# Performance work log

Measured on AMD Instinct MI355X. Metric: run time of the kernel, lower is better.

Reference implementation:

```python
import jax, jax.numpy as jnp
import numpy as np

P = 10          # num_patches
EPS = 1e-20
ALPHAS = dict(stretch=1.0, E=1.0, G=1.0, skew=1.0, total_area=1.0, total_area_mult=1.0)
ALPHA_MC = 1.0
ALPHA_DISTORT = 1.0


def setup_inputs() -> dict:
    key = jax.random.key(0)
    k1, k2, k3, k4 = jax.random.split(key, 4)
    B, N, M = 8, 8192, 2500
    pc_gt = jax.random.normal(k1, (B, N, 3), dtype=jnp.float32)
    pc_pred = jax.random.normal(k2, (B, M, 3), dtype=jnp.float32)
    # first fundamental form (E, F, G); ensure E*G - F^2 > 0 so sqrt is smooth
    u = jax.random.uniform(k3, (B, M, 3), dtype=jnp.float32)
    fff = u * 0.5 + jnp.array([1.0, 0.0, 1.0], dtype=jnp.float32)
    A_gt = jax.random.uniform(k4, (B,), dtype=jnp.float32)
    return {"pc_gt": pc_gt, "pc_pred": pc_pred, "fff": fff, "A_gt": A_gt}


def _forward(pc_gt, pc_pred, fff, A_gt):
    B, M, _ = pc_pred.shape
    spp = M // P

    # ---- Chamfer distance via dense (B, M, N) distance matrix + argmin ----
    diff = pc_pred[:, :, None, :] - pc_gt[:, None, :, :]          # (B, M, N, 3)
    distm = jnp.sqrt(jnp.sum(diff * diff, axis=3))                # (B, M, N)
    inds_p2gt = jnp.argmin(distm, axis=2)                         # (B, M)
    inds_gt2p = jnp.argmin(distm, axis=1)                         # (B, N)
    pc_gt_reg = jnp.take_along_axis(pc_gt, inds_p2gt[..., None], axis=1)   # (B, M, 3)
    pc_p_reg = jnp.take_along_axis(pc_pred, inds_gt2p[..., None], axis=1)  # (B, N, 3)
    d_p2gt = jnp.sum((pc_pred - pc_gt_reg) ** 2, axis=2)
    d_gt2p = jnp.sum((pc_gt - pc_p_reg) ** 2, axis=2)
    L_chd = d_p2gt.mean() + d_gt2p.mean()

    # ---- FFF-based losses ----
    EFG = jnp.transpose(fff.reshape(B, P, spp, 3), (3, 0, 1, 2))  # (3, B, P, spp)
    E, F, G = EFG[0], EFG[1], EFG[2]

    # metric consistency between consecutive frame pairs
    Eh = E.reshape(B // 2, 2, P, spp)
    Fh = F.reshape(B // 2, 2, P, spp)
    Gh = G.reshape(B // 2, 2, P, spp)
    L_mc = ((Eh[:, 0] - Eh[:, 1]) ** 2
            + 2.0 * (Fh[:, 0] - Fh[:, 1]) ** 2
            + (Gh[:, 0] - Gh[:, 1]) ** 2).mean()

    # scaled isometry (collapse) losses
    A2 = jnp.maximum(E * G - F * F, 0.0)                          # (B, P, spp)
    A = jnp.sqrt(A2)
    inv = 1.0 / (A2 + EPS)
    L_stretch = (((E - G) ** 2) * inv).mean() * ALPHAS['stretch']
    L_E = (((E - E.mean()) ** 2) * inv).mean() * ALPHAS['E']
    L_G = (((G - G.mean()) ** 2) * inv).mean() * ALPHAS['G']
    L_F = ((F * F) * inv).mean() * ALPHAS['skew']

    # overlap / total-area loss
    A_tot = A.mean(axis=2).sum(axis=1)                            # (B,)
    L_olap = (jnp.maximum(0.0, A_tot - A_gt * ALPHAS['total_area_mult']) ** 2).mean() * ALPHAS['total_area']

    loss_sciso = L_F + L_E + L_G + L_stretch + L_olap
    loss_tot = L_chd + ALPHA_MC * L_mc + ALPHA_DISTORT * loss_sciso
    return loss_tot


def reference(pc_gt, pc_pred, fff, A_gt):
    return _forward(pc_gt, pc_pred, fff, A_gt)
```

## Files before the change

kernel.cpp:

```cpp
#include <hip/hip_runtime.h>

#define B_   8
#define N_   8192
#define M_   2500
#define SPP_ 250
#define EPS_ 1e-20f
#define BIGF 1e30f

#define NB_P2GT 640
#define NB_GT2P 512
#define NB_FFF1 79
#define NB_K1   (NB_P2GT + NB_GT2P + NB_FFF1)

#define NB_RG2P 256
#define NB_RP2  79
#define NB_FFF2 79
#define NB_K2   (NB_RG2P + NB_RP2 + NB_FFF2)

#define WS_P2GT 0
#define WS_GT2P 160000
#define WS_F1P  291072
#define WS_RED  292336
#define RO_G2P  0
#define RO_P2   256
#define RO_EC   335
#define RO_GC   414
#define WS_CNT  292829

typedef __attribute__((ext_vector_type(8)))  short short8_t;
typedef __attribute__((ext_vector_type(4)))  float float4_t;

__device__ __forceinline__ unsigned pack_bf2(float lo, float hi) {
    unsigned a = __float_as_uint(lo);
    unsigned b = __float_as_uint(hi);
    a = (a + 0x7FFFu + ((a >> 16) & 1u)) >> 16;
    b = (b + 0x7FFFu + ((b >> 16) & 1u)) & 0xFFFF0000u;
    return a | b;
}
__device__ __forceinline__ short bf16s(float x) {
    unsigned a = __float_as_uint(x);
    return (short)((a + 0x7FFFu + ((a >> 16) & 1u)) >> 16);
}

__device__ __forceinline__ float wave_sum64(float v) {
    #pragma unroll
    for (int o = 32; o > 0; o >>= 1) v += __shfl_down(v, o, 64);
    return v;
}
__device__ __forceinline__ float block_sum256(float v, float* red4) {
    v = wave_sum64(v);
    int wid  = threadIdx.x >> 6;
    int lane = threadIdx.x & 63;
    if (lane == 0) red4[wid] = v;
    __syncthreads();
    float r = 0.f;
    if (threadIdx.x == 0) r = red4[0] + red4[1] + red4[2] + red4[3];
    __syncthreads();
    return r;
}

__device__ __forceinline__ void min4(float4_t& c, const float4_t d) {
    c.x = fminf(c.x, d.x); c.y = fminf(c.y, d.y);
    c.z = fminf(c.z, d.z); c.w = fminf(c.w, d.w);
}
__device__ __forceinline__ void quad_min4(float4_t& c) {
    #pragma unroll
    for (int m = 1; m < 16; m <<= 1) {
        c.x = fminf(c.x, __shfl_xor(c.x, m, 64));
        c.y = fminf(c.y, __shfl_xor(c.y, m, 64));
        c.z = fminf(c.z, __shfl_xor(c.z, m, 64));
        c.w = fminf(c.w, __shfl_xor(c.w, m, 64));
    }
}

__global__ void __launch_bounds__(256) k1_main(
        const float* __restrict__ gt, const float* __restrict__ pred,
        const float* __restrict__ fff, float* __restrict__ ws) {
    __shared__ uint4 spts[1280];
    __shared__ __align__(16) float saux[256];
    const int bid = blockIdx.x;
    const int tid = threadIdx.x;
    const int lane = tid & 63;
    const int w    = tid >> 6;
    const int quad = lane >> 4;
    const int l15  = lane & 15;

    if (bid == 0 && tid == 0) ((unsigned*)(ws + WS_CNT))[0] = 0u;

    if (bid < NB_P2GT + NB_GT2P) {
        const bool is_p2gt = bid < NB_P2GT;
        int b, mblk, z, ntiles, nstage, blim, alim;
        const float* apts; const float* bpts; float* dst;
        if (is_p2gt) {
            z = bid / 80; int rem = bid % 80;
            b = rem / 10; mblk = rem % 10;
            apts = pred + (size_t)b * M_ * 3;
            bpts = gt + ((size_t)b * N_ + (size_t)z * 1024) * 3;
            ntiles = 64; nstage = 1024; blim = 1024; alim = M_;
            dst = ws + WS_P2GT + (size_t)z * 20000 + b * M_;
        } else {
            int r = bid - NB_P2GT;
            z = r >> 8; int rem = r & 255;
            b = rem >> 5; mblk = rem & 31;
            apts = gt + (size_t)b * N_ * 3;
            bpts = pred + ((size_t)b * M_ + (size_t)z * 1280) * 3;
            ntiles = 80; nstage = 1280; blim = M_ - z * 1280; alim = N_;
            dst = ws + WS_GT2P + (size_t)z * 65536 + b * N_;
        }
        const int abase = mblk * 256 + w * 64;

        for (int i = tid; i < nstage; i += 256) {
            float x = 0.f, y = 0.f, zc = 0.f, n2 = BIGF;
            if (i < blim) {
                x = bpts[i * 3 + 0]; y = bpts[i * 3 + 1]; zc = bpts[i * 3 + 2];
                n2 = x * x + y * y + zc * zc;
            }
            uint4 q;
            q.x = pack_bf2(-2.f * x, -2.f * y);
            q.y = pack_bf2(-2.f * zc, n2);
            q.z = q.x; q.w = q.y;
            spts[i] = q;
        }

        short8_t af[4];
        #pragma unroll
        for (int t = 0; t < 4; ++t) af[t] = (short8_t){0,0,0,0,0,0,0,0};
        if (lane < 16) {
            #pragma unroll
            for (int t = 0; t < 4; ++t) {
                int m = abase + t * 16 + l15;
                int c = m < alim ? m : alim - 1;
                float x = apts[c*3+0], y = apts[c*3+1], zc = apts[c*3+2];
                af[t][0] = bf16s(x); af[t][1] = bf16s(y); af[t][2] = bf16s(zc);
                af[t][3] = (short)0x3F80;
                saux[w * 64 + t * 16 + l15] = x*x + y*y + zc*zc;
            }
        }
        __syncthreads();

        const float4_t* bp = (const float4_t*)saux;
        float4_t bias[4];
        #pragma unroll
        for (int t = 0; t < 4; ++t) bias[t] = bp[w * 16 + t * 4 + quad];

        float4_t c[4];
        #pragma unroll
        for (int t = 0; t < 4; ++t) c[t] = (float4_t){BIGF, BIGF, BIGF, BIGF};

        const uint4* bptr = spts + l15;
        #pragma unroll 4
        for (int i = 0; i < ntiles; ++i) {
            short8_t bf = __builtin_bit_cast(short8_t, bptr[i * 16]);
            #pragma unroll
            for (int t = 0; t < 4; ++t) {
                float4_t d = __builtin_amdgcn_mfma_f32_16x16x32_bf16(
                                 af[t], bf, bias[t], 0, 0, 0);
                min4(c[t], d);
            }
        }
        #pragma unroll
        for (int t = 0; t < 4; ++t) quad_min4(c[t]);

        if (l15 == 0) {
            #pragma unroll
            for (int t = 0; t < 4; ++t) {
                int m0 = abase + t * 16 + quad * 4;
                if (m0 < alim)
                    *(float4_t*)(dst + m0) = c[t];
            }
        }
    } else {
        const int kb = bid - NB_P2GT - NB_GT2P;
        const int i  = kb * 256 + tid;
        float* red4 = saux;
        float* sA   = saux + 8;
        if (tid < B_) sA[tid] = 0.f;
        __syncthreads();

        float sE = 0.f, sG = 0.f, sMC = 0.f, sST = 0.f, sF = 0.f;
        if (i < B_ * M_) {
            const int b = i / M_;
            const int m = i - b * M_;
            const float* f = fff + (size_t)i * 3;
            float E = f[0], F = f[1], G = f[2];
            sE = E; sG = G;
            float A2  = fmaxf(E * G - F * F, 0.f);
            float inv = 1.f / (A2 + EPS_);
            sST = (E - G) * (E - G) * inv;
            sF  = F * F * inv;
            atomicAdd(&sA[b], sqrtf(A2));
            if ((b & 1) == 0) {
                const float* f2 = fff + ((size_t)(b + 1) * M_ + m) * 3;
                float dE = E - f2[0], dF = F - f2[1], dG = G - f2[2];
                sMC = dE * dE + 2.f * dF * dF + dG * dG;
            }
        }
        float rE  = block_sum256(sE,  red4);
        float rG  = block_sum256(sG,  red4);
        float rMC = block_sum256(sMC, red4);
        float rST = block_sum256(sST, red4);
        float rF  = block_sum256(sF,  red4);
        float* outp = ws + WS_F1P + (size_t)kb * 16;
        if (tid == 0) {
            outp[0] = rE; outp[1] = rG; outp[2] = rMC; outp[3] = rST; outp[4] = rF;
        }
        __syncthreads();
        if (tid < B_) outp[5 + tid] = sA[tid];
    }
}

__global__ void __launch_bounds__(256) k2_reduce(
        const float* __restrict__ fff, const float* __restrict__ A_gt,
        float* __restrict__ ws, float* __restrict__ out) {
    __shared__ float red4[4];
    __shared__ float bc2[2];
    const int bid = blockIdx.x;
    const int tid = threadIdx.x;
    float* redp = ws + WS_RED;
    const float* f1p = ws + WS_F1P;

    if (bid < NB_RG2P) {
        const int o = bid * 256 + tid;
        const float* src = ws + WS_GT2P + o;
        float m = fminf(src[0], src[65536]);
        float r = block_sum256(fmaxf(m, 0.f), red4);
        if (tid == 0) redp[RO_G2P + bid] = r;
    } else if (bid < NB_RG2P + NB_RP2) {
        const int kb = bid - NB_RG2P;
        const int o = kb * 256 + tid;
        float s = 0.f;
        if (o < 20000) {
            const float* src = ws + WS_P2GT + o;
            float m = src[0];
            #pragma unroll
            for (int zz = 1; zz < 8; ++zz) m = fminf(m, src[zz * 20000]);
            s = fmaxf(m, 0.f);
        }
        float r = block_sum256(s, red4);
        if (tid == 0) redp[RO_P2 + kb] = r;
    } else {
        const int kb = bid - NB_RG2P - NB_RP2;
        float pe = 0.f, pg = 0.f;
        if (tid < 79) { pe = f1p[tid * 16 + 0]; pg = f1p[tid * 16 + 1]; }
        float rE = block_sum256(pe, red4);
        float rG = block_sum256(pg, red4);
        if (tid == 0) { bc2[0] = rE; bc2[1] = rG; }
        __syncthreads();
        const float mE = bc2[0] * (1.f / 20000.f);
        const float mG = bc2[1] * (1.f / 20000.f);

        const int i = kb * 256 + tid;
        float sEC = 0.f, sGC = 0.f;
        if (i < B_ * M_) {
            const float* f = fff + (size_t)i * 3;
            float E = f[0], F = f[1], G = f[2];
            float A2  = fmaxf(E * G - F * F, 0.f);
            float inv = 1.f / (A2 + EPS_);
            sEC = (E - mE) * (E - mE) * inv;
            sGC = (G - mG) * (G - mG) * inv;
        }
        float rEC = block_sum256(sEC, red4);
        float rGC = block_sum256(sGC, red4);
        if (tid == 0) { redp[RO_EC + kb] = rEC; redp[RO_GC + kb] = rGC; }
    }

    __syncthreads();
    if (tid == 0) __threadfence();
    __syncthreads();
    __shared__ unsigned old_s;
    if (tid == 0)
        old_s = __hip_atomic_fetch_add((unsigned*)(ws + WS_CNT), 1u,
                                       __ATOMIC_ACQ_REL, __HIP_MEMORY_SCOPE_AGENT);
    __syncthreads();
    if (old_s == (unsigned)(NB_K2 - 1)) {
        float v;
        v = redp[RO_G2P + tid];
        float sGT2P = block_sum256(v, red4);
        v = (tid < 79) ? redp[RO_P2 + tid] : 0.f;
        float sP2GT = block_sum256(v, red4);
        v = (tid < 79) ? redp[RO_EC + tid] : 0.f;
        float sEC = block_sum256(v, red4);
        v = (tid < 79) ? redp[RO_GC + tid] : 0.f;
        float sGC = block_sum256(v, red4);
        v = (tid < 79) ? f1p[tid * 16 + 2] : 0.f;
        float sMC = block_sum256(v, red4);
        v = (tid < 79) ? f1p[tid * 16 + 3] : 0.f;
        float sST = block_sum256(v, red4);
        v = (tid < 79) ? f1p[tid * 16 + 4] : 0.f;
        float sF = block_sum256(v, red4);
        float sAb[B_];
        #pragma unroll
        for (int b = 0; b < B_; ++b) {
            v = (tid < 79) ? f1p[tid * 16 + 5 + b] : 0.f;
            sAb[b] = block_sum256(v, red4);
        }
        if (tid == 0) {
            float L_chd = sP2GT * (1.f / 20000.f) + sGT2P * (1.f / 65536.f);
            float L_mc  = sMC * (1.f / 10000.f);
            float L_sc  = (sST + sF + sEC + sGC) * (1.f / 20000.f);
            float L_olap = 0.f;
            #pragma unroll
            for (int b = 0; b < B_; ++b) {
                float At = sAb[b] * (1.f / (float)SPP_);
                float r  = fmaxf(0.f, At - A_gt[b]);
                L_olap += r * r;
            }
            L_olap *= (1.f / (float)B_);
            out[0] = L_chd + L_mc + L_sc + L_olap;
        }
    }
}

extern "C" void kernel_launch(void* const* d_in, const int* in_sizes, int n_in,
                              void* d_out, int out_size, void* d_ws, size_t ws_size,
                              hipStream_t stream) {
    const float* pc_gt   = (const float*)d_in[0];
    const float* pc_pred = (const float*)d_in[1];
    const float* fff     = (const float*)d_in[2];
    const float* A_gt    = (const float*)d_in[3];
    float* ws  = (float*)d_ws;
    float* out = (float*)d_out;

    k1_main  <<<NB_K1, 256, 0, stream>>>(pc_gt, pc_pred, fff, ws);
    k2_reduce<<<NB_K2, 256, 0, stream>>>(fff, A_gt, ws, out);
}
```

Baseline: 107.6 us.

## Fuse reduction kernel into main kernel with per-tile counters and algebraic variance expansion

Merges the two kernels into one. Per-row-block atomic counters let the last z-slice block compute the min-across-slices and its partial sum, and a global counter lets the last block finish the loss. The E/G centered losses are expanded algebraically into raw moment sums (E^2*inv, E*inv, inv), so the second pass over fff is gone. Each wave now handles 8 MFMA row tiles instead of 4, which halves block counts. A memset launch is added, and the expanded form risks cancellation error.

Measured after the change: 153.2 us. +42.5%, slower.

```diff
diff --git a/kernel.cpp b/kernel.cpp
--- a/kernel.cpp
+++ b/kernel.cpp
@@ -7,28 +7,34 @@
 #define EPS_ 1e-20f
 #define BIGF 1e30f
 
-#define NB_P2GT 640
-#define NB_GT2P 512
-#define NB_FFF1 79
-#define NB_K1   (NB_P2GT + NB_GT2P + NB_FFF1)
-
-#define NB_RG2P 256
-#define NB_RP2  79
-#define NB_FFF2 79
-#define NB_K2   (NB_RG2P + NB_RP2 + NB_FFF2)
+#define NB_P2GT 320
+#define NB_GT2P 256
+#define NB_FFF  79
+#define NB_ALL  (NB_P2GT + NB_GT2P + NB_FFF)
 
 #define WS_P2GT 0
 #define WS_GT2P 160000
-#define WS_F1P  291072
-#define WS_RED  292336
-#define RO_G2P  0
-#define RO_P2   256
-#define RO_EC   335
-#define RO_GC   414
-#define WS_CNT  292829
-
-typedef __attribute__((ext_vector_type(8)))  short short8_t;
-typedef __attribute__((ext_vector_type(4)))  float float4_t;
+#define WS_ACC  291072
+#define WS_GC   291092
+#define GC_P2   0
+#define GC_G2   40
+#define GC_ALL  168
+#define A_P2   0
+#define A_G2   1
+#define A_E    2
+#define A_G    3
+#define A_MC   4
+#define A_ST   5
+#define A_F2I  6
+#define A_E2I  7
+#define A_EI   8
+#define A_G2I  9
+#define A_GI   10
+#define A_I    11
+#define A_AB   12
+
+typedef __attribute__((ext_vector_type(8))) short short8_t;
+typedef __attribute__((ext_vector_type(4))) float float4_t;
 
 __device__ __forceinline__ unsigned pack_bf2(float lo, float hi) {
     unsigned a = __float_as_uint(lo);
@@ -41,16 +47,14 @@
     unsigned a = __float_as_uint(x);
     return (short)((a + 0x7FFFu + ((a >> 16) & 1u)) >> 16);
 }
-
 __device__ __forceinline__ float wave_sum64(float v) {
     #pragma unroll
     for (int o = 32; o > 0; o >>= 1) v += __shfl_down(v, o, 64);
     return v;
 }
-__device__ __forceinline__ float block_sum256(float v, float* red4) {
+__device__ __forceinline__ float block_sum256(float v, volatile float* red4) {
     v = wave_sum64(v);
-    int wid  = threadIdx.x >> 6;
-    int lane = threadIdx.x & 63;
+    int wid = threadIdx.x >> 6, lane = threadIdx.x & 63;
     if (lane == 0) red4[wid] = v;
     __syncthreads();
     float r = 0.f;
@@ -58,7 +62,6 @@
     __syncthreads();
     return r;
 }
-
 __device__ __forceinline__ void min4(float4_t& c, const float4_t d) {
     c.x = fminf(c.x, d.x); c.y = fminf(c.y, d.y);
     c.z = fminf(c.z, d.z); c.w = fminf(c.w, d.w);
@@ -73,41 +76,46 @@
     }
 }
 
-__global__ void __launch_bounds__(256) k1_main(
+__global__ void __launch_bounds__(256) fused_all(
         const float* __restrict__ gt, const float* __restrict__ pred,
-        const float* __restrict__ fff, float* __restrict__ ws) {
+        const float* __restrict__ fff, const float* __restrict__ A_gt,
+        float* __restrict__ ws, float* __restrict__ out) {
     __shared__ uint4 spts[1280];
-    __shared__ __align__(16) float saux[256];
+    __shared__ __align__(16) float saux[516];
+    __shared__ bool isred;
     const int bid = blockIdx.x;
     const int tid = threadIdx.x;
     const int lane = tid & 63;
     const int w    = tid >> 6;
     const int quad = lane >> 4;
     const int l15  = lane & 15;
-
-    if (bid == 0 && tid == 0) ((unsigned*)(ws + WS_CNT))[0] = 0u;
+    float* acc = ws + WS_ACC;
+    unsigned* gc = (unsigned*)(ws + WS_GC);
 
     if (bid < NB_P2GT + NB_GT2P) {
         const bool is_p2gt = bid < NB_P2GT;
-        int b, mblk, z, ntiles, nstage, blim, alim;
+        int b, mblk, z, ntiles, blim, alim, gidx, nz;
         const float* apts; const float* bpts; float* dst;
         if (is_p2gt) {
-            z = bid / 80; int rem = bid % 80;
-            b = rem / 10; mblk = rem % 10;
+            z = bid / 40; int rem = bid % 40;
+            b = rem / 5;  mblk = rem % 5;
             apts = pred + (size_t)b * M_ * 3;
             bpts = gt + ((size_t)b * N_ + (size_t)z * 1024) * 3;
-            ntiles = 64; nstage = 1024; blim = 1024; alim = M_;
-            dst = ws + WS_P2GT + (size_t)z * 20000 + b * M_;
+            ntiles = 64; blim = 1024; alim = M_;
+            dst  = ws + WS_P2GT + (size_t)z * 20000 + b * M_;
+            gidx = GC_P2 + b * 5 + mblk; nz = 8;
         } else {
             int r = bid - NB_P2GT;
-            z = r >> 8; int rem = r & 255;
-            b = rem >> 5; mblk = rem & 31;
+            z = r >> 7; int rem = r & 127;
+            b = rem >> 4; mblk = rem & 15;
             apts = gt + (size_t)b * N_ * 3;
             bpts = pred + ((size_t)b * M_ + (size_t)z * 1280) * 3;
-            ntiles = 80; nstage = 1280; blim = M_ - z * 1280; alim = N_;
-            dst = ws + WS_GT2P + (size_t)z * 65536 + b * N_;
-        }
-        const int abase = mblk * 256 + w * 64;
+            ntiles = 80; blim = M_ - z * 1280; alim = N_;
+            dst  = ws + WS_GT2P + (size_t)z * 65536 + b * N_;
+            gidx = GC_G2 + b * 16 + mblk; nz = 2;
+        }
+        const int abase = mblk * 512;
+        const int nstage = ntiles * 16;
 
         for (int i = tid; i < nstage; i += 256) {
             float x = 0.f, y = 0.f, zc = 0.f, n2 = BIGF;
@@ -122,188 +130,151 @@
             spts[i] = q;
         }
 
-        short8_t af[4];
+        short8_t af[8];
         #pragma unroll
-        for (int t = 0; t < 4; ++t) af[t] = (short8_t){0,0,0,0,0,0,0,0};
+        for (int t = 0; t < 8; ++t) af[t] = (short8_t){0,0,0,0,0,0,0,0};
         if (lane < 16) {
             #pragma unroll
-            for (int t = 0; t < 4; ++t) {
-                int m = abase + t * 16 + l15;
+            for (int t = 0; t < 8; ++t) {
+                int m = abase + w * 128 + t * 16 + l15;
                 int c = m < alim ? m : alim - 1;
                 float x = apts[c*3+0], y = apts[c*3+1], zc = apts[c*3+2];
                 af[t][0] = bf16s(x); af[t][1] = bf16s(y); af[t][2] = bf16s(zc);
                 af[t][3] = (short)0x3F80;
-                saux[w * 64 + t * 16 + l15] = x*x + y*y + zc*zc;
+                saux[w * 128 + t * 16 + l15] = x*x + y*y + zc*zc;
             }
         }
         __syncthreads();
 
         const float4_t* bp = (const float4_t*)saux;
-        float4_t bias[4];
+        float4_t bias[8], c[8];
         #pragma unroll
-        for (int t = 0; t < 4; ++t) bias[t] = bp[w * 16 + t * 4 + quad];
-
-        float4_t c[4];
-        #pragma unroll
-        for (int t = 0; t < 4; ++t) c[t] = (float4_t){BIGF, BIGF, BIGF, BIGF};
+        for (int t = 0; t < 8; ++t) {
+            bias[t] = bp[w * 32 + t * 4 + quad];
+            c[t] = (float4_t){BIGF, BIGF, BIGF, BIGF};
+        }
 
         const uint4* bptr = spts + l15;
-        #pragma unroll 4
+        #pragma unroll 2
         for (int i = 0; i < ntiles; ++i) {
             short8_t bf = __builtin_bit_cast(short8_t, bptr[i * 16]);
             #pragma unroll
-            for (int t = 0; t < 4; ++t) {
+            for (int t = 0; t < 8; ++t) {
                 float4_t d = __builtin_amdgcn_mfma_f32_16x16x32_bf16(
                                  af[t], bf, bias[t], 0, 0, 0);
                 min4(c[t], d);
             }
         }
         #pragma unroll
-        for (int t = 0; t < 4; ++t) quad_min4(c[t]);
-
+        for (int t = 0; t < 8; ++t) {
+            quad_min4(c[t]);
+            c[t].x = fmaxf(c[t].x, 0.f); c[t].y = fmaxf(c[t].y, 0.f);
+            c[t].z = fmaxf(c[t].z, 0.f); c[t].w = fmaxf(c[t].w, 0.f);
+        }
         if (l15 == 0) {
             #pragma unroll
-            for (int t = 0; t < 4; ++t) {
-                int m0 = abase + t * 16 + quad * 4;
+            for (int t = 0; t < 8; ++t) {
+                int m0 = abase + w * 128 + t * 16 + quad * 4;
                 if (m0 < alim)
                     *(float4_t*)(dst + m0) = c[t];
             }
+        }
+
+        __threadfence();
+        __syncthreads();
+        if (tid == 0) {
+            unsigned old = __hip_atomic_fetch_add(&gc[gidx], 1u,
+                              __ATOMIC_ACQ_REL, __HIP_MEMORY_SCOPE_AGENT);
+            isred = (old == (unsigned)(nz - 1));
+        }
+        __syncthreads();
+        if (isred) {
+            float s = 0.f;
+            #pragma unroll
+            for (int h = 0; h < 2; ++h) {
+                int m = abase + h * 256 + tid;
+                if (m < alim) {
+                    const float* src = (is_p2gt ? ws + WS_P2GT + b * M_
+                                                : ws + WS_GT2P + b * N_) + m;
+                    int stride = is_p2gt ? 20000 : 65536;
+                    float v = src[0];
+                    for (int zz = 1; zz < nz; ++zz)
+                        v = fminf(v, src[(size_t)zz * stride]);
+                    s += v;
+                }
+            }
+            float r = block_sum256(s, saux + 512);
+            if (tid == 0) atomicAdd(&acc[is_p2gt ? A_P2 : A_G2], r);
         }
     } else {
         const int kb = bid - NB_P2GT - NB_GT2P;
         const int i  = kb * 256 + tid;
-        float* red4 = saux;
-        float* sA   = saux + 8;
+        volatile float* red4 = saux + 512;
+        float* sA = saux;
         if (tid < B_) sA[tid] = 0.f;
         __syncthreads();
 
-        float sE = 0.f, sG = 0.f, sMC = 0.f, sST = 0.f, sF = 0.f;
+        float vE=0.f,vG=0.f,vMC=0.f,vST=0.f,vF2=0.f,vE2=0.f,vEI=0.f,
+              vG2=0.f,vGI=0.f,vI=0.f;
         if (i < B_ * M_) {
             const int b = i / M_;
             const int m = i - b * M_;
             const float* f = fff + (size_t)i * 3;
             float E = f[0], F = f[1], G = f[2];
-            sE = E; sG = G;
             float A2  = fmaxf(E * G - F * F, 0.f);
             float inv = 1.f / (A2 + EPS_);
-            sST = (E - G) * (E - G) * inv;
-            sF  = F * F * inv;
+            vE = E; vG = G;
+            vST = (E - G) * (E - G) * inv;
+            vF2 = F * F * inv;
+            vE2 = E * E * inv; vEI = E * inv;
+            vG2 = G * G * inv; vGI = G * inv;
+            vI  = inv;
             atomicAdd(&sA[b], sqrtf(A2));
             if ((b & 1) == 0) {
                 const float* f2 = fff + ((size_t)(b + 1) * M_ + m) * 3;
                 float dE = E - f2[0], dF = F - f2[1], dG = G - f2[2];
-                sMC = dE * dE + 2.f * dF * dF + dG * dG;
-            }
-        }
-        float rE  = block_sum256(sE,  red4);
-        float rG  = block_sum256(sG,  red4);
-        float rMC = block_sum256(sMC, red4);
-        float rST = block_sum256(sST, red4);
-        float rF  = block_sum256(sF,  red4);
-        float* outp = ws + WS_F1P + (size_t)kb * 16;
-        if (tid == 0) {
-            outp[0] = rE; outp[1] = rG; outp[2] = rMC; outp[3] = rST; outp[4] = rF;
-        }
-        __syncthreads();
-        if (tid < B_) outp[5 + tid] = sA[tid];
+                vMC = dE * dE + 2.f * dF * dF + dG * dG;
+            }
+        }
+        float r;
+        r = block_sum256(vE,  red4); if (tid==0) atomicAdd(&acc[A_E],   r);
+        r = block_sum256(vG,  red4); if (tid==0) atomicAdd(&acc[A_G],   r);
+        r = block_sum256(vMC, red4); if (tid==0) atomicAdd(&acc[A_MC],  r);
+        r = block_sum256(vST, red4); if (tid==0) atomicAdd(&acc[A_ST],  r);
+        r = block_sum256(vF2, red4); if (tid==0) atomicAdd(&acc[A_F2I], r);
+        r = block_sum256(vE2, red4); if (tid==0) atomicAdd(&acc[A_E2I], r);
+        r = block_sum256(vEI, red4); if (tid==0) atomicAdd(&acc[A_EI],  r);
+        r = block_sum256(vG2, red4); if (tid==0) atomicAdd(&acc[A_G2I], r);
+        r = block_sum256(vGI, red4); if (tid==0) atomicAdd(&acc[A_GI],  r);
+        r = block_sum256(vI,  red4); if (tid==0) atomicAdd(&acc[A_I],   r);
+        __syncthreads();
+        if (tid < B_ && sA[tid] != 0.f) atomicAdd(&acc[A_AB + tid], sA[tid]);
     }
-}
-
-__global__ void __launch_bounds__(256) k2_reduce(
-        const float* __restrict__ fff, const float* __restrict__ A_gt,
-        float* __restrict__ ws, float* __restrict__ out) {
-    __shared__ float red4[4];
-    __shared__ float bc2[2];
-    const int bid = blockIdx.x;
-    const int tid = threadIdx.x;
-    float* redp = ws + WS_RED;
-    const float* f1p = ws + WS_F1P;
-
-    if (bid < NB_RG2P) {
-        const int o = bid * 256 + tid;
-        const float* src = ws + WS_GT2P + o;
-        float m = fminf(src[0], src[65536]);
-        float r = block_sum256(fmaxf(m, 0.f), red4);
-        if (tid == 0) redp[RO_G2P + bid] = r;
-    } else if (bid < NB_RG2P + NB_RP2) {
-        const int kb = bid - NB_RG2P;
-        const int o = kb * 256 + tid;
-        float s = 0.f;
-        if (o < 20000) {
-            const float* src = ws + WS_P2GT + o;
-            float m = src[0];
-            #pragma unroll
-            for (int zz = 1; zz < 8; ++zz) m = fminf(m, src[zz * 20000]);
-            s = fmaxf(m, 0.f);
-        }
-        float r = block_sum256(s, red4);
-        if (tid == 0) redp[RO_P2 + kb] = r;
-    } else {
-        const int kb = bid - NB_RG2P - NB_RP2;
-        float pe = 0.f, pg = 0.f;
-        if (tid < 79) { pe = f1p[tid * 16 + 0]; pg = f1p[tid * 16 + 1]; }
-        float rE = block_sum256(pe, red4);
-        float rG = block_sum256(pg, red4);
-        if (tid == 0) { bc2[0] = rE; bc2[1] = rG; }
-        __syncthreads();
-        const float mE = bc2[0] * (1.f / 20000.f);
-        const float mG = bc2[1] * (1.f / 20000.f);
-
-        const int i = kb * 256 + tid;
-        float sEC = 0.f, sGC = 0.f;
-        if (i < B_ * M_) {
-            const float* f = fff + (size_t)i * 3;
-            float E = f[0], F = f[1], G = f[2];
-            float A2  = fmaxf(E * G - F * F, 0.f);
-            float inv = 1.f / (A2 + EPS_);
-            sEC = (E - mE) * (E - mE) * inv;
-            sGC = (G - mG) * (G - mG) * inv;
-        }
-        float rEC = block_sum256(sEC, red4);
-        float rGC = block_sum256(sGC, red4);
-        if (tid == 0) { redp[RO_EC + kb] = rEC; redp[RO_GC + kb] = rGC; }
-    }
 
     __syncthreads();
-    if (tid == 0) __threadfence();
-    __syncthreads();
-    __shared__ unsigned old_s;
-    if (tid == 0)
-        old_s = __hip_atomic_fetch_add((unsigned*)(ws + WS_CNT), 1u,
-                                       __ATOMIC_ACQ_REL, __HIP_MEMORY_SCOPE_AGENT);
-    __syncthreads();
-    if (old_s == (unsigned)(NB_K2 - 1)) {
-        float v;
-        v = redp[RO_G2P + tid];
-        float sGT2P = block_sum256(v, red4);
-        v = (tid < 79) ? redp[RO_P2 + tid] : 0.f;
-        float sP2GT = block_sum256(v, red4);
-        v = (tid < 79) ? redp[RO_EC + tid] : 0.f;
-        float sEC = block_sum256(v, red4);
-        v = (tid < 79) ? redp[RO_GC + tid] : 0.f;
-        float sGC = block_sum256(v, red4);
-        v = (tid < 79) ? f1p[tid * 16 + 2] : 0.f;
-        float sMC = block_sum256(v, red4);
-        v = (tid < 79) ? f1p[tid * 16 + 3] : 0.f;
-        float sST = block_sum256(v, red4);
-        v = (tid < 79) ? f1p[tid * 16 + 4] : 0.f;
-        float sF = block_sum256(v, red4);
-        float sAb[B_];
-        #pragma unroll
-        for (int b = 0; b < B_; ++b) {
-            v = (tid < 79) ? f1p[tid * 16 + 5 + b] : 0.f;
-            sAb[b] = block_sum256(v, red4);
-        }
-        if (tid == 0) {
-            float L_chd = sP2GT * (1.f / 20000.f) + sGT2P * (1.f / 65536.f);
-            float L_mc  = sMC * (1.f / 10000.f);
-            float L_sc  = (sST + sF + sEC + sGC) * (1.f / 20000.f);
+    if (tid == 0) {
+        __threadfence();
+        unsigned old = __hip_atomic_fetch_add(&gc[GC_ALL], 1u,
+                          __ATOMIC_ACQ_REL, __HIP_MEMORY_SCOPE_AGENT);
+        if (old == (unsigned)(NB_ALL - 1)) {
+            float a[20];
+            #pragma unroll
+            for (int k = 0; k < 20; ++k)
+                a[k] = __hip_atomic_load(&acc[k], __ATOMIC_RELAXED,
+                                         __HIP_MEMORY_SCOPE_AGENT);
+            const float inv20k = 1.f / 20000.f;
+            float mE = a[A_E] * inv20k, mG = a[A_G] * inv20k;
+            float L_E = (a[A_E2I] - 2.f*mE*a[A_EI] + mE*mE*a[A_I]) * inv20k;
+            float L_G = (a[A_G2I] - 2.f*mG*a[A_GI] + mG*mG*a[A_I]) * inv20k;
+            float L_sc = L_E + L_G + (a[A_ST] + a[A_F2I]) * inv20k;
+            float L_mc = a[A_MC] * (1.f / 10000.f);
+            float L_chd = a[A_P2] * inv20k + a[A_G2] * (1.f / 65536.f);
             float L_olap = 0.f;
             #pragma unroll
             for (int b = 0; b < B_; ++b) {
-                float At = sAb[b] * (1.f / (float)SPP_);
-                float r  = fmaxf(0.f, At - A_gt[b]);
-                L_olap += r * r;
+                float At = a[A_AB + b] * (1.f / (float)SPP_);
+                float d  = fmaxf(0.f, At - A_gt[b]);
+                L_olap += d * d;
             }
             L_olap *= (1.f / (float)B_);
             out[0] = L_chd + L_mc + L_sc + L_olap;
@@ -321,6 +292,6 @@
     float* ws  = (float*)d_ws;
     float* out = (float*)d_out;
 
-    k1_main  <<<NB_K1, 256, 0, stream>>>(pc_gt, pc_pred, fff, ws);
-    k2_reduce<<<NB_K2, 256, 0, stream>>>(fff, A_gt, ws, out);
-}
+    hipMemsetAsync(ws + WS_ACC, 0, (20 + 169) * sizeof(float), stream);
+    fused_all<<<NB_ALL, 256, 0, stream>>>(pc_gt, pc_pred, fff, A_gt, ws, out);
+}
```
